# Kernel tuning notes

Hardware: AMD Instinct MI355X
Metric: run time of the kernel (lower is better)

Reference implementation:

```python
import jax, jax.numpy as jnp
import numpy as np

B, T, E, H, ENC, V = 32, 128, 256, 512, 512, 10000


def setup_inputs() -> dict:
    key = jax.random.key(0)
    ks = jax.random.split(key, 16)
    s = 0.02
    return {
        "text_vectors": jax.random.normal(ks[0], (B, ENC), dtype=jnp.float32),
        "texts": jax.random.randint(ks[1], (B, T), 0, V),
        "lengths": jax.random.randint(ks[2], (B,), 1, T + 1),
        "start_idx": 1,
        "emb_table": jax.random.normal(ks[3], (V, E), dtype=jnp.float32) * s,
        "W_ih": jax.random.normal(ks[4], (4 * H, E + H + ENC), dtype=jnp.float32) * s,
        "b_ih": jnp.zeros((4 * H,), dtype=jnp.float32),
        "W_hh": jax.random.normal(ks[5], (4 * H, H), dtype=jnp.float32) * s,
        "b_hh": jnp.zeros((4 * H,), dtype=jnp.float32),
        "Wo_w": jax.random.normal(ks[6], (H, ENC), dtype=jnp.float32) * s,
        "Wo_b": jnp.zeros((H,), dtype=jnp.float32),
        "Wh_w": jax.random.normal(ks[7], (H, ENC), dtype=jnp.float32) * s,
        "Wh_b": jnp.zeros((H,), dtype=jnp.float32),
        "Wc_w": jax.random.normal(ks[8], (H, ENC), dtype=jnp.float32) * s,
        "Wc_b": jnp.zeros((H,), dtype=jnp.float32),
        "Wv_w": jax.random.normal(ks[9], (V, H), dtype=jnp.float32) * s,
        "Wv_b": jnp.zeros((V,), dtype=jnp.float32),
    }


def reference(text_vectors, texts, lengths, start_idx, emb_table,
              W_ih, b_ih, W_hh, b_hh, Wo_w, Wo_b, Wh_w, Wh_b, Wc_w, Wc_b,
              Wv_w, Wv_b):
    del lengths  # unused in the original forward loop
    batch = texts.shape[0]
    # initial previous-token embedding = embedding of start token, broadcast
    y0 = jnp.broadcast_to(emb_table[start_idx], (batch, emb_table.shape[1]))
    o = text_vectors @ Wo_w.T + Wo_b          # [B, H], constant across steps
    h0 = text_vectors @ Wh_w.T + Wh_b          # [B, H]
    c0 = text_vectors @ Wc_w.T + Wc_b          # [B, H]
    embedded_texts = emb_table[texts.T]        # [T, B, E]

    def step(carry, emb_t):
        h, c, y = carry
        x = jnp.concatenate((y, o, text_vectors), axis=1)  # [B, E+H+ENC]
        gates = x @ W_ih.T + b_ih + h @ W_hh.T + b_hh      # [B, 4H]
        i_g, f_g, g_g, o_g = jnp.split(gates, 4, axis=1)
        c = jax.nn.sigmoid(f_g) * c + jax.nn.sigmoid(i_g) * jnp.tanh(g_g)
        h = jax.nn.sigmoid(o_g) * jnp.tanh(c)
        return (h, c, emb_t), h

    _, hs = jax.lax.scan(step, (h0, c0, y0), embedded_texts)  # hs: [T, B, H]
    logits = jnp.einsum('tbh,vh->btv', hs, Wv_w) + Wv_b        # [B, T, V]
    return logits
```

## Files before the change

kernel.cpp:

```cpp
#include <hip/hip_runtime.h>
#include <math.h>

#define Bx   32
#define Tx   128
#define Ex   256
#define Hx   512
#define ENCx 512
#define Vx   10000
#define G4   2048

#define RBLK 64
#define UPB  8
#define KREC 768
#define KPAD 776

typedef __bf16 bf16x8 __attribute__((ext_vector_type(8)));
typedef float  f32x4  __attribute__((ext_vector_type(4)));

#define MFMA16 __builtin_amdgcn_mfma_f32_16x16x32_bf16

__device__ __forceinline__ float sigm(float x) { return 1.0f / (1.0f + expf(-x)); }

__device__ __forceinline__ void store_u32_wt(uint32_t* p, uint32_t v) {
  asm volatile("global_store_dword %0, %1, off sc0 sc1" :: "v"(p), "v"(v) : "memory");
}
__device__ __forceinline__ uint32_t load_u32_coh(const uint32_t* p) {
  uint32_t v;
  asm volatile("global_load_dword %0, %1, off sc0 sc1\n\ts_waitcnt vmcnt(0)"
               : "=v"(v) : "v"(p) : "memory");
  return v;
}

__global__ __launch_bounds__(256) void k_init(
    const float* __restrict__ tv,
    const float* __restrict__ Wo_w, const float* __restrict__ Wo_b,
    const float* __restrict__ Wh_w, const float* __restrict__ Wh_b,
    const float* __restrict__ Wc_w, const float* __restrict__ Wc_b,
    float* __restrict__ o, __bf16* __restrict__ hinit, float* __restrict__ c0) {
  int tid = blockIdx.x * blockDim.x + threadIdx.x;
  int which = tid / (Bx * Hx);
  int r = tid - which * (Bx * Hx);
  int b = r >> 9, j = r & (Hx - 1);
  const float* W; const float* bias;
  if (which == 0)      { W = Wo_w; bias = Wo_b; }
  else if (which == 1) { W = Wh_w; bias = Wh_b; }
  else                 { W = Wc_w; bias = Wc_b; }
  const float* x = tv + b * ENCx;
  const float* w = W + (size_t)j * ENCx;
  float acc = bias[j];
#pragma unroll 8
  for (int k = 0; k < ENCx; k++) acc += x[k] * w[k];
  if (which == 0)      o[b * Hx + j] = acc;
  else if (which == 1) hinit[b * Hx + j] = (__bf16)acc;
  else                 c0[j * Bx + b] = acc;
}

__global__ __launch_bounds__(256) void k_const(
    const float* __restrict__ tv, const float* __restrict__ o,
    const float* __restrict__ W_ih, const float* __restrict__ b_ih,
    const float* __restrict__ b_hh, float* __restrict__ constC,
    int* __restrict__ flags) {
  int tid = blockIdx.x * blockDim.x + threadIdx.x;
  if (tid < RBLK) flags[tid] = 0;
  int b = tid >> 11, g = tid & (G4 - 1);
  const float* w = W_ih + (size_t)g * (Ex + Hx + ENCx);
  float acc = b_ih[g] + b_hh[g];
  const float* ob = o + b * Hx;
#pragma unroll 8
  for (int k = 0; k < Hx; k++) acc += ob[k] * w[Ex + k];
  const float* xb = tv + b * ENCx;
#pragma unroll 8
  for (int k = 0; k < ENCx; k++) acc += xb[k] * w[Ex + Hx + k];
  constC[b * G4 + g] = acc;
}

__global__ __launch_bounds__(256) void k_cvt(
    const float* __restrict__ src, __bf16* __restrict__ dst, int n) {
  int i = (blockIdx.x * blockDim.x + threadIdx.x) * 4;
  if (i < n) {
    float4 v = *(const float4*)(src + i);
    dst[i + 0] = (__bf16)v.x; dst[i + 1] = (__bf16)v.y;
    dst[i + 2] = (__bf16)v.z; dst[i + 3] = (__bf16)v.w;
  }
}

__global__ __launch_bounds__(256) void k_cvt2d(
    const float* __restrict__ src, __bf16* __restrict__ dst) {
  int idx = (blockIdx.x * 256 + threadIdx.x) * 4;
  int row = idx >> 8, col = idx & 255;
  float4 v = *(const float4*)(src + (size_t)row * 1280 + col);
  dst[idx + 0] = (__bf16)v.x; dst[idx + 1] = (__bf16)v.y;
  dst[idx + 2] = (__bf16)v.z; dst[idx + 3] = (__bf16)v.w;
}

__global__ __launch_bounds__(256) void k_rec(
    const __bf16* __restrict__ Whb,
    const __bf16* __restrict__ Wihb,
    const __bf16* __restrict__ embb,
    const int* __restrict__ texts, const int* __restrict__ sidx,
    const float* __restrict__ constC,
    const float* __restrict__ c0,
    const __bf16* __restrict__ hinit,
    __bf16* __restrict__ hs2,
    int* __restrict__ flags) {
  __shared__ __bf16 Ws[2 * 16][KPAD];
  __shared__ __bf16 Hs[32][KPAD];
  __shared__ float  Cs[32][33];
  __shared__ float  CsC[32][33];
  __shared__ __bf16 Ht[32][8];
  __shared__ int    tokL[Bx * Tx];

  const int q = threadIdx.x;
  const int nb = blockIdx.x;
  const int u0 = nb * UPB;
  const int lane = q & 63, wave = q >> 6;
  const int mt = wave & 1, jt = wave >> 1;
  const int fm = lane & 15, fk = (lane >> 4) * 8;
  const int cr = (lane >> 4) * 4, cc = lane & 15;
  const int s0tok = sidx[0];

  {
    const int row = q >> 3;
    const int wr = (row & 3) * Hx + u0 + (row >> 2);
    const __bf16* wh = Whb + (size_t)wr * Hx;
    const __bf16* wy = Wihb + (size_t)wr * Ex;
#pragma unroll
    for (int r = 0; r < 12; r++) {
      const int col = ((q & 7) + 8 * r) * 8;
      bf16x8 v = (col < Hx) ? *(const bf16x8*)(wh + col)
                            : *(const bf16x8*)(wy + col - Hx);
      *(bf16x8*)&Ws[row][col] = v;
    }
  }
#pragma unroll
  for (int r = 0; r < 16; r++) tokL[q + 256 * r] = texts[q + 256 * r];
#pragma unroll
  for (int r = 0; r < 4; r++) {
    const int idx = q + 256 * r;
    const int b = idx >> 5, n = idx & 31;
    CsC[b][n] = constC[b * G4 + (n & 3) * Hx + u0 + (n >> 2)];
  }
#pragma unroll
  for (int r = 0; r < 4; r++) {
    const int vy = q + 256 * r;
    const int row = vy >> 5, col = (vy & 31) * 8;
    *(bf16x8*)&Hs[row][Hx + col] = *(const bf16x8*)(embb + (size_t)s0tok * Ex + col);
  }

  const int eb = q & 31, eu = q >> 5, eu4 = (q >> 5) * 4;
  float creg = c0[(u0 + eu) * Bx + eb];

  for (int t = 0; t < Tx; t++) {
    {
      const __bf16* hsrc = (t == 0) ? hinit : hs2 + (size_t)(t - 1) * (Bx * Hx);
      bf16x8 hv[8];
#pragma unroll
      for (int r = 0; r < 8; r++) {
        const int hi = q + 256 * r;
        const __bf16* p = hsrc + (hi >> 6) * Hx + (hi & 63) * 8;
        asm volatile("global_load_dwordx4 %0, %1, off sc0 sc1"
                     : "=v"(hv[r]) : "v"(p) : "memory");
      }
      asm volatile("s_waitcnt vmcnt(0)" ::: "memory");
      __builtin_amdgcn_sched_barrier(0);
#pragma unroll
      for (int r = 0; r < 8; r++) {
        const int hi = q + 256 * r;
        *(bf16x8*)&Hs[hi >> 6][(hi & 63) * 8] = hv[r];
      }
    }
    __syncthreads();

    f32x4 accA = {0.f, 0.f, 0.f, 0.f}, accB = {0.f, 0.f, 0.f, 0.f};
    const __bf16* ha = &Hs[mt * 16 + fm][0];
    const __bf16* wrow = &Ws[jt * 16 + fm][0];
#pragma unroll
    for (int ks = 0; ks < 24; ks += 2) {
      accA = MFMA16(*(const bf16x8*)(ha + ks * 32 + fk),
                    *(const bf16x8*)(wrow + ks * 32 + fk), accA, 0, 0, 0);
      accB = MFMA16(*(const bf16x8*)(ha + ks * 32 + 32 + fk),
                    *(const bf16x8*)(wrow + ks * 32 + 32 + fk), accB, 0, 0, 0);
    }
    {
      const f32x4 acc = accA + accB;
#pragma unroll
      for (int r = 0; r < 4; r++) Cs[mt * 16 + cr + r][jt * 16 + cc] = acc[r];
    }
    __syncthreads();

    bf16x8 yv[4];
    const int tn = t + 1;
    if (tn < Tx) {
#pragma unroll
      for (int r = 0; r < 4; r++) {
        const int vy = q + 256 * r;
        const int row = vy >> 5, col = (vy & 31) * 8;
        const int tok = tokL[row * Tx + tn - 1];
        yv[r] = *(const bf16x8*)(embb + (size_t)tok * Ex + col);
      }
    }
    {
      const float pi = Cs[eb][eu4 + 0] + CsC[eb][eu4 + 0];
      const float pf = Cs[eb][eu4 + 1] + CsC[eb][eu4 + 1];
      const float pg = Cs[eb][eu4 + 2] + CsC[eb][eu4 + 2];
      const float po = Cs[eb][eu4 + 3] + CsC[eb][eu4 + 3];
      const float cn = sigm(pf) * creg + sigm(pi) * tanhf(pg);
      creg = cn;
      Ht[eb][eu] = (__bf16)(sigm(po) * tanhf(cn));
    }
    if (tn < Tx) {
#pragma unroll
      for (int r = 0; r < 4; r++) {
        const int vy = q + 256 * r;
        const int row = vy >> 5, col = (vy & 31) * 8;
        *(bf16x8*)&Hs[row][Hx + col] = yv[r];
      }
    }
    __syncthreads();

    if (wave == 0) {
      uint32_t* dst = (uint32_t*)(hs2 + (size_t)t * (Bx * Hx));
#pragma unroll
      for (int r = 0; r < 2; r++) {
        const int idx = lane + 64 * r;
        const int b = idx >> 2, dw = idx & 3;
        const uint32_t val = *(const uint32_t*)&Ht[b][dw * 2];
        store_u32_wt(dst + (size_t)b * (Hx / 2) + (u0 >> 1) + dw, val);
      }
      asm volatile("s_waitcnt vmcnt(0)" ::: "memory");
      if (lane == 0 && t < Tx - 1)
        store_u32_wt((uint32_t*)&flags[nb], (uint32_t)(t + 1));
    } else if (wave == 1 && t < Tx - 1) {
      if (lane != nb) {
        while ((int)load_u32_coh((const uint32_t*)&flags[lane]) < t + 1)
          __builtin_amdgcn_s_sleep(1);
      }
    }
    __syncthreads();
  }
}

#define PM 128
#define PN 128
#define PK 32
#define PKP 40

__global__ __launch_bounds__(256) void k_proj_mfma(
    const __bf16* __restrict__ A,
    const __bf16* __restrict__ Bw,
    const float* __restrict__ bias, float* __restrict__ C) {
  __shared__ __bf16 As[PM][PKP];
  __shared__ __bf16 Bs[PN][PKP];
  const int m0 = blockIdx.x * PM;
  const int n0 = blockIdx.y * PN;
  const int t = threadIdx.x;
  const int wave = t >> 6, lane = t & 63;
  const int wm = (wave & 1) * 64, wn = (wave >> 1) * 64;
  const int fm = lane & 15, fk = (lane >> 4) * 8;
  const int sr = t >> 2, sk = (t & 3) * 8;

  const int n1 = min(n0 + sr, Vx - 1);
  const int n2 = min(n0 + sr + 64, Vx - 1);
  const int g1 = m0 + sr, g2 = m0 + sr + 64;
  const int r1 = ((g1 & 127) << 5) | (g1 >> 7);
  const int r2 = ((g2 & 127) << 5) | (g2 >> 7);

  f32x4 acc[4][4];
#pragma unroll
  for (int i = 0; i < 4; i++)
#pragma unroll
    for (int j = 0; j < 4; j++) acc[i][j] = (f32x4){0.f, 0.f, 0.f, 0.f};

  for (int k0 = 0; k0 < Hx; k0 += PK) {
    __syncthreads();
    *(bf16x8*)&As[sr][sk]      = *(const bf16x8*)&A[(size_t)r1 * Hx + k0 + sk];
    *(bf16x8*)&As[sr + 64][sk] = *(const bf16x8*)&A[(size_t)r2 * Hx + k0 + sk];
    *(bf16x8*)&Bs[sr][sk]      = *(const bf16x8*)&Bw[(size_t)n1 * Hx + k0 + sk];
    *(bf16x8*)&Bs[sr + 64][sk] = *(const bf16x8*)&Bw[(size_t)n2 * Hx + k0 + sk];
    __syncthreads();
    bf16x8 af[4], bfr[4];
#pragma unroll
    for (int i = 0; i < 4; i++) af[i]  = *(const bf16x8*)&As[wm + i * 16 + fm][fk];
#pragma unroll
    for (int j = 0; j < 4; j++) bfr[j] = *(const bf16x8*)&Bs[wn + j * 16 + fm][fk];
#pragma unroll
    for (int i = 0; i < 4; i++)
#pragma unroll
      for (int j = 0; j < 4; j++)
        acc[i][j] = MFMA16(af[i], bfr[j], acc[i][j], 0, 0, 0);
  }

  const int cr = (lane >> 4) * 4, cc = lane & 15;
#pragma unroll
  for (int i = 0; i < 4; i++) {
#pragma unroll
    for (int r = 0; r < 4; r++) {
      const int m = m0 + wm + i * 16 + cr + r;
      float* crow = C + (size_t)m * Vx;
#pragma unroll
      for (int j = 0; j < 4; j++) {
        const int n = n0 + wn + j * 16 + cc;
        if (n < Vx) crow[n] = acc[i][j][r] + bias[n];
      }
    }
  }
}

extern "C" void kernel_launch(void* const* d_in, const int* in_sizes, int n_in,
                              void* d_out, int out_size, void* d_ws, size_t ws_size,
                              hipStream_t stream) {
  const float* tv     = (const float*)d_in[0];
  const int*   texts  = (const int*)d_in[1];
  const int*   sidx   = (const int*)d_in[3];
  const float* emb    = (const float*)d_in[4];
  const float* W_ih   = (const float*)d_in[5];
  const float* b_ih   = (const float*)d_in[6];
  const float* W_hh   = (const float*)d_in[7];
  const float* b_hh   = (const float*)d_in[8];
  const float* Wo_w   = (const float*)d_in[9];
  const float* Wo_b   = (const float*)d_in[10];
  const float* Wh_w   = (const float*)d_in[11];
  const float* Wh_b   = (const float*)d_in[12];
  const float* Wc_w   = (const float*)d_in[13];
  const float* Wc_b   = (const float*)d_in[14];
  const float* Wv_w   = (const float*)d_in[15];
  const float* Wv_b   = (const float*)d_in[16];
  float* out = (float*)d_out;

  float* ws     = (float*)d_ws;
  float* o      = ws;
  float* c0     = o + Bx * Hx;
  float* constC = c0 + Hx * Bx;
  int*   flags  = (int*)(constC + (size_t)Bx * G4);
  __bf16* bfb   = (__bf16*)(ws + 98816);
  __bf16* hinit = bfb;
  __bf16* hs2   = hinit + Bx * Hx;
  __bf16* Wvb   = hs2 + (size_t)Bx * Tx * Hx;
  __bf16* Whb   = Wvb + (size_t)Vx * Hx;
  __bf16* embb  = Whb + (size_t)G4 * Hx;
  __bf16* Wihb  = embb + (size_t)Vx * Ex;

  hipLaunchKernelGGL(k_cvt, dim3((Vx * Hx / 4 + 255) / 256), dim3(256), 0, stream,
                     Wv_w, Wvb, Vx * Hx);
  hipLaunchKernelGGL(k_cvt, dim3((G4 * Hx / 4 + 255) / 256), dim3(256), 0, stream,
                     W_hh, Whb, G4 * Hx);
  hipLaunchKernelGGL(k_cvt, dim3((Vx * Ex / 4 + 255) / 256), dim3(256), 0, stream,
                     emb, embb, Vx * Ex);
  hipLaunchKernelGGL(k_cvt2d, dim3(G4 * Ex / 4 / 256), dim3(256), 0, stream,
                     W_ih, Wihb);
  hipLaunchKernelGGL(k_init, dim3(192), dim3(256), 0, stream,
                     tv, Wo_w, Wo_b, Wh_w, Wh_b, Wc_w, Wc_b, o, hinit, c0);
  hipLaunchKernelGGL(k_const, dim3(256), dim3(256), 0, stream,
                     tv, o, W_ih, b_ih, b_hh, constC, flags);
  hipLaunchKernelGGL(k_rec, dim3(RBLK), dim3(256), 0, stream,
                     Whb, Wihb, embb, texts, sidx, constC, c0, hinit, hs2, flags);
  hipLaunchKernelGGL(k_proj_mfma, dim3((Bx * Tx) / PM, (Vx + PN - 1) / PN), dim3(256), 0, stream,
                     hs2, Wvb, Wv_b, out);
}
```

Baseline: 1.001 ms.

## Overlap per-block flag polling with incremental hidden-state gathers in recurrence

The recurrent kernel no longer waits for every block's flag and then reloads the full hidden state at the start of each step. Each wave now polls a group of 16 producer flags and loads the matching hidden-state slices into shared memory as soon as both blocks of a pair are ready. Each thread writes its own bf16 hidden value straight to global memory, which drops the Ht staging buffer, and the constant gate terms now live in registers instead of shared memory. The aim is to shorten the cross-block synchronisation gap on the serial critical path, at the cost of more complex polling logic and many small narrow global stores.

```diff
diff --git a/kernel.cpp b/kernel.cpp
--- a/kernel.cpp
+++ b/kernel.cpp
@@ -24,11 +24,8 @@
 __device__ __forceinline__ void store_u32_wt(uint32_t* p, uint32_t v) {
   asm volatile("global_store_dword %0, %1, off sc0 sc1" :: "v"(p), "v"(v) : "memory");
 }
-__device__ __forceinline__ uint32_t load_u32_coh(const uint32_t* p) {
-  uint32_t v;
-  asm volatile("global_load_dword %0, %1, off sc0 sc1\n\ts_waitcnt vmcnt(0)"
-               : "=v"(v) : "v"(p) : "memory");
-  return v;
+__device__ __forceinline__ void store_b16_wt(__bf16* p, uint32_t v) {
+  asm volatile("global_store_short %0, %1, off sc0 sc1" :: "v"(p), "v"(v) : "memory");
 }
 
 __global__ __launch_bounds__(256) void k_init(
@@ -106,8 +103,6 @@
   __shared__ __bf16 Ws[2 * 16][KPAD];
   __shared__ __bf16 Hs[32][KPAD];
   __shared__ float  Cs[32][33];
-  __shared__ float  CsC[32][33];
-  __shared__ __bf16 Ht[32][8];
   __shared__ int    tokL[Bx * Tx];
 
   const int q = threadIdx.x;
@@ -135,10 +130,10 @@
 #pragma unroll
   for (int r = 0; r < 16; r++) tokL[q + 256 * r] = texts[q + 256 * r];
 #pragma unroll
-  for (int r = 0; r < 4; r++) {
-    const int idx = q + 256 * r;
-    const int b = idx >> 5, n = idx & 31;
-    CsC[b][n] = constC[b * G4 + (n & 3) * Hx + u0 + (n >> 2)];
+  for (int r = 0; r < 8; r++) {
+    const int hv = q + 256 * r;
+    const int row = hv >> 6, col = (hv & 63) * 8;
+    *(bf16x8*)&Hs[row][col] = *(const bf16x8*)(hinit + row * Hx + col);
   }
 #pragma unroll
   for (int r = 0; r < 4; r++) {
@@ -147,30 +142,16 @@
     *(bf16x8*)&Hs[row][Hx + col] = *(const bf16x8*)(embb + (size_t)s0tok * Ex + col);
   }
 
-  const int eb = q & 31, eu = q >> 5, eu4 = (q >> 5) * 4;
+  const int eb = q >> 3, eu = q & 7, eu4 = (q & 7) * 4;
   float creg = c0[(u0 + eu) * Bx + eb];
+  const float cc0v = constC[eb * G4 + 0 * Hx + u0 + eu];
+  const float cc1v = constC[eb * G4 + 1 * Hx + u0 + eu];
+  const float cc2v = constC[eb * G4 + 2 * Hx + u0 + eu];
+  const float cc3v = constC[eb * G4 + 3 * Hx + u0 + eu];
+
+  __syncthreads();
 
   for (int t = 0; t < Tx; t++) {
-    {
-      const __bf16* hsrc = (t == 0) ? hinit : hs2 + (size_t)(t - 1) * (Bx * Hx);
-      bf16x8 hv[8];
-#pragma unroll
-      for (int r = 0; r < 8; r++) {
-        const int hi = q + 256 * r;
-        const __bf16* p = hsrc + (hi >> 6) * Hx + (hi & 63) * 8;
-        asm volatile("global_load_dwordx4 %0, %1, off sc0 sc1"
-                     : "=v"(hv[r]) : "v"(p) : "memory");
-      }
-      asm volatile("s_waitcnt vmcnt(0)" ::: "memory");
-      __builtin_amdgcn_sched_barrier(0);
-#pragma unroll
-      for (int r = 0; r < 8; r++) {
-        const int hi = q + 256 * r;
-        *(bf16x8*)&Hs[hi >> 6][(hi & 63) * 8] = hv[r];
-      }
-    }
-    __syncthreads();
-
     f32x4 accA = {0.f, 0.f, 0.f, 0.f}, accB = {0.f, 0.f, 0.f, 0.f};
     const __bf16* ha = &Hs[mt * 16 + fm][0];
     const __bf16* wrow = &Ws[jt * 16 + fm][0];
@@ -200,13 +181,15 @@
       }
     }
     {
-      const float pi = Cs[eb][eu4 + 0] + CsC[eb][eu4 + 0];
-      const float pf = Cs[eb][eu4 + 1] + CsC[eb][eu4 + 1];
-      const float pg = Cs[eb][eu4 + 2] + CsC[eb][eu4 + 2];
-      const float po = Cs[eb][eu4 + 3] + CsC[eb][eu4 + 3];
+      const float pi = Cs[eb][eu4 + 0] + cc0v;
+      const float pf = Cs[eb][eu4 + 1] + cc1v;
+      const float pg = Cs[eb][eu4 + 2] + cc2v;
+      const float po = Cs[eb][eu4 + 3] + cc3v;
       const float cn = sigm(pf) * creg + sigm(pi) * tanhf(pg);
       creg = cn;
-      Ht[eb][eu] = (__bf16)(sigm(po) * tanhf(cn));
+      const __bf16 hb = (__bf16)(sigm(po) * tanhf(cn));
+      const uint32_t hu = (uint32_t)__builtin_bit_cast(unsigned short, hb);
+      store_b16_wt(hs2 + (size_t)t * (Bx * Hx) + eb * Hx + u0 + eu, hu);
     }
     if (tn < Tx) {
 #pragma unroll
@@ -216,24 +199,52 @@
         *(bf16x8*)&Hs[row][Hx + col] = yv[r];
       }
     }
-    __syncthreads();
-
-    if (wave == 0) {
-      uint32_t* dst = (uint32_t*)(hs2 + (size_t)t * (Bx * Hx));
-#pragma unroll
-      for (int r = 0; r < 2; r++) {
-        const int idx = lane + 64 * r;
-        const int b = idx >> 2, dw = idx & 3;
-        const uint32_t val = *(const uint32_t*)&Ht[b][dw * 2];
-        store_u32_wt(dst + (size_t)b * (Hx / 2) + (u0 >> 1) + dw, val);
-      }
-      asm volatile("s_waitcnt vmcnt(0)" ::: "memory");
-      if (lane == 0 && t < Tx - 1)
-        store_u32_wt((uint32_t*)&flags[nb], (uint32_t)(t + 1));
-    } else if (wave == 1 && t < Tx - 1) {
-      if (lane != nb) {
-        while ((int)load_u32_coh((const uint32_t*)&flags[lane]) < t + 1)
-          __builtin_amdgcn_s_sleep(1);
+    asm volatile("s_waitcnt vmcnt(0)" ::: "memory");
+    __syncthreads();
+
+    if (t < Tx - 1) {
+      if (q == 0) store_u32_wt((uint32_t*)&flags[nb], t + 1);
+      const __bf16* src = hs2 + (size_t)t * (Bx * Hx);
+      const int sbase = wave * 16;
+      const int myfl = (nb >= sbase && nb < sbase + 16) ? (nb - sbase) : -1;
+      const int prow = lane >> 1, phalf = lane & 1;
+      bf16x8 pv0, pv1, pv2, pv3, pv4, pv5, pv6, pv7;
+      uint32_t done = 0, prevm = 0;
+      for (;;) {
+        uint32_t fv = 0;
+        const bool last = ((done | prevm) == 0xFFu);
+        if (!last && lane < 16) {
+          if (lane == myfl) {
+            fv = 0x7FFFFFFFu;
+          } else {
+            const uint32_t* fp = (const uint32_t*)&flags[sbase + lane];
+            asm volatile("global_load_dword %0, %1, off sc0 sc1"
+                         : "=v"(fv) : "v"(fp));
+          }
+        }
+        asm volatile("s_waitcnt vmcnt(0)" ::: "memory");
+        __builtin_amdgcn_sched_barrier(0);
+#define WR_P(P) if (prevm & (1u << P)) \
+  *(bf16x8*)&Hs[prow][(sbase + 2 * P) * 8 + phalf * 8] = pv##P;
+        WR_P(0) WR_P(1) WR_P(2) WR_P(3) WR_P(4) WR_P(5) WR_P(6) WR_P(7)
+#undef WR_P
+        done |= prevm;
+        if (done == 0xFFu) break;
+        const bool rdy = (lane < 16) && ((int)fv >= t + 1);
+        const unsigned long long bl = __ballot(rdy);
+        const uint32_t r16 = (uint32_t)bl & 0xFFFFu;
+        const uint32_t x = r16 & (r16 >> 1);
+        const uint32_t pairm = (x & 1u) | ((x >> 1) & 2u) | ((x >> 2) & 4u)
+                             | ((x >> 3) & 8u) | ((x >> 4) & 16u)
+                             | ((x >> 5) & 32u) | ((x >> 6) & 64u)
+                             | ((x >> 7) & 128u);
+        const uint32_t newm = pairm & ~done;
+        prevm = newm;
+#define LD_P(P) if (newm & (1u << P)) { \
+  const __bf16* p_ = src + prow * Hx + (sbase + 2 * P) * 8 + phalf * 8; \
+  asm volatile("global_load_dwordx4 %0, %1, off sc0 sc1" : "=v"(pv##P) : "v"(p_)); }
+        LD_P(0) LD_P(1) LD_P(2) LD_P(3) LD_P(4) LD_P(5) LD_P(6) LD_P(7)
+#undef LD_P
       }
     }
     __syncthreads();
```

Measured after the change: 975.4 us. 2.6% less time.
